# Kernel tuning notes

Hardware: AMD Instinct MI355X
Metric: run time of the kernel (lower is better)

The kernel has to match this reference:

```python
import jax, jax.numpy as jnp
import numpy as np

NUM_TILES = 64
TPC = 8            # tiles per cluster
GRID = 16          # spline grid size
EPS = 1e-5


def setup_inputs() -> dict:
    key = jax.random.key(0)
    ks = jax.random.split(key, 6)
    B, S, D, T, DH, G = 2, 1024, 512, NUM_TILES, 128, GRID
    x = jax.random.normal(ks[0], (B, S, D), dtype=jnp.float32)
    gamma = jnp.ones((D,), jnp.float32)
    beta = jnp.zeros((D,), jnp.float32)
    # torch layouts: down.weight [DH, D], up.weight [D, DH]
    Wd = jax.random.normal(ks[1], (T, DH, D), dtype=jnp.float32) * 0.02
    spline_bases = jax.random.normal(ks[2], (T, DH, G), dtype=jnp.float32) * 0.1
    spline_slopes = jax.random.normal(ks[3], (T, DH, G), dtype=jnp.float32) * 0.1
    Wu = jax.random.normal(ks[4], (T, D, DH), dtype=jnp.float32) * 0.02
    scale = jnp.full((T,), 0.1, jnp.float32)
    return {"x": x, "gamma": gamma, "beta": beta, "Wd": Wd,
            "spline_bases": spline_bases, "spline_slopes": spline_slopes,
            "Wu": Wu, "scale": scale}


def reference(x, gamma, beta, Wd, spline_bases, spline_slopes, Wu, scale):
    B, S, D = x.shape
    T, DH, _ = Wd.shape
    C = T // TPC
    N = B * S

    # LayerNorm
    mu = x.mean(-1, keepdims=True)
    var = ((x - mu) ** 2).mean(-1, keepdims=True)
    xn = (x - mu) * jax.lax.rsqrt(var + EPS) * gamma + beta
    xf = xn.reshape(N, D)

    # Signatures (first call: ema == current tile signatures)
    tile_sigs = jnp.sign(Wd.mean(axis=1))                         # [T, D]
    cluster_sigs = jnp.sign(tile_sigs.reshape(C, TPC, D).mean(1))  # [C, D]

    # Hierarchical routing: cluster -> tile
    in_sigs = jnp.sign(xf)                                        # [N, D]
    best_c = jnp.argmax(in_sigs @ cluster_sigs.T, axis=-1)        # [N]
    tile_scores = (in_sigs @ tile_sigs.T).reshape(N, C, TPC)      # [N, C, TPC]
    sc = jnp.take_along_axis(tile_scores, best_c[:, None, None], axis=1)[:, 0, :]
    local_best = jnp.argmax(sc, axis=-1)                          # [N]
    tidx = best_c * TPC + local_best                              # [N]

    # Dispatch: gather per-token expert weights, down-project
    h = jnp.einsum('nd,nhd->nh', xf, Wd[tidx])                    # [N, DH]

    # Spline nonlinearity
    hn = jax.nn.sigmoid(h)
    idx = jnp.clip((hn * GRID).astype(jnp.int32), 0, GRID - 1)    # [N, DH]
    base = jnp.take_along_axis(spline_bases[tidx], idx[..., None], axis=-1)[..., 0]
    slope = jnp.take_along_axis(spline_slopes[tidx], idx[..., None], axis=-1)[..., 0]
    local_pos = hn * GRID - idx.astype(h.dtype)                   # (hn - idx*cell)/cell
    hs = base + slope * local_pos                                 # [N, DH]

    # Up-project, per-tile scale, combine (dropout is identity in eval)
    y = jnp.einsum('nh,ndh->nd', hs, Wu[tidx]) * scale[tidx][:, None]
    return x + y.reshape(B, S, D)
```

## Files before the change

### kernel.cpp

```cpp
#include <hip/hip_runtime.h>
#include <hip/hip_bf16.h>
#include <math.h>

#define NTILES 64
#define TPC 8
#define NCLUST 8
#define GRID_SZ 16
#define DIM 512
#define DHID 128
#define NTOK 2048
#define LN_EPS 1e-5f
#define TB 16
#define NCHUNK_MAX 192

typedef __attribute__((ext_vector_type(8))) short bf16x8;
typedef __attribute__((ext_vector_type(4))) float f32x4;

static __device__ __forceinline__ float fsign(float v) {
    return (v > 0.f) ? 1.f : ((v < 0.f) ? -1.f : 0.f);
}

static __device__ __forceinline__ unsigned short bf16bits(float f) {
    union { __hip_bfloat16 h; unsigned short s; } u;
    u.h = __float2bfloat16(f);
    return u.s;
}

static __device__ __forceinline__ bf16x8 cvt8(const float* p) {
    float4 a = *(const float4*)p;
    float4 b = *(const float4*)(p + 4);
    float e[8] = {a.x, a.y, a.z, a.w, b.x, b.y, b.z, b.w};
    bf16x8 v;
    #pragma unroll
    for (int i = 0; i < 8; ++i) v[i] = (short)bf16bits(e[i]);
    return v;
}

static __device__ __forceinline__ bool route_chunk(const int* counts, int lane, int cb,
                                                   int& t, int& base, int& m) {
    int cnt_l = counts[lane];
    int nck = (cnt_l + TB - 1) / TB;
    int pre = nck;
    #pragma unroll
    for (int off = 1; off < 64; off <<= 1) {
        int u = __shfl_up(pre, off);
        if (lane >= off) pre += u;
    }
    int total = __shfl(pre, 63);
    pre -= nck;
    if (cb >= total) return false;
    unsigned long long msk = __ballot(cb >= pre && cb < pre + nck);
    t = (int)__builtin_ctzll(msk);
    base = (cb - __shfl(pre, t)) * TB;
    m = min(TB, __shfl(cnt_l, t) - base);
    return true;
}

__global__ __launch_bounds__(256) void k_prep(const float* __restrict__ x,
                                              const float* __restrict__ gamma,
                                              const float* __restrict__ beta,
                                              const float* __restrict__ Wd,
                                              float* __restrict__ psum,
                                              unsigned short* __restrict__ wd_b,
                                              unsigned short* __restrict__ xn_b,
                                              int* __restrict__ counts) {
    int bid = blockIdx.x;
    int tid = threadIdx.x;
    if (bid < 512) {
        int t = bid >> 3, part = bid & 7;
        const float* basep = Wd + ((size_t)t * DHID + part * 16) * DIM;
        unsigned short* bb = wd_b + ((size_t)t * DHID + part * 16) * DIM;
        #pragma unroll
        for (int k2 = 0; k2 < 2; ++k2) {
            int d = tid + k2 * 256;
            float s = 0.f;
            #pragma unroll
            for (int j = 0; j < 16; ++j) {
                float v = basep[(size_t)j * DIM + d];
                s += v;
                bb[(size_t)j * DIM + d] = bf16bits(v);
            }
            psum[((size_t)t * 8 + part) * DIM + d] = s;
        }
        if (bid == 0 && tid < NTILES) counts[tid] = 0;
    } else {
        int n = (bid - 512) * 4 + (tid >> 6);
        int lane = tid & 63;
        const float* xr = x + (size_t)n * DIM;
        float v[8];
        float sum = 0.f;
        #pragma unroll
        for (int j = 0; j < 8; ++j) { float t = xr[lane + 64 * j]; v[j] = t; sum += t; }
        #pragma unroll
        for (int off = 32; off; off >>= 1) sum += __shfl_xor(sum, off);
        float mu = sum * (1.f / DIM);
        float sq = 0.f;
        #pragma unroll
        for (int j = 0; j < 8; ++j) { float t = v[j] - mu; sq += t * t; }
        #pragma unroll
        for (int off = 32; off; off >>= 1) sq += __shfl_xor(sq, off);
        float rs = rsqrtf(sq * (1.f / DIM) + LN_EPS);
        #pragma unroll
        for (int j = 0; j < 8; ++j) {
            int d = lane + 64 * j;
            float xv = (v[j] - mu) * rs * gamma[d] + beta[d];
            xn_b[(size_t)n * DIM + d] = bf16bits(xv);
        }
    }
}

__global__ __launch_bounds__(512) void k_csig(const float* __restrict__ psum,
                                              float* __restrict__ tile_sigs,
                                              float* __restrict__ cluster_sigs) {
    int c = blockIdx.x, d = threadIdx.x;
    float csum = 0.f;
    #pragma unroll
    for (int k = 0; k < TPC; ++k) {
        int t = c * TPC + k;
        float s = 0.f;
        #pragma unroll
        for (int p = 0; p < 8; ++p) s += psum[((size_t)t * 8 + p) * DIM + d];
        float sg = fsign(s);
        tile_sigs[(size_t)t * DIM + d] = sg;
        csum += sg;
    }
    cluster_sigs[(size_t)c * DIM + d] = fsign(csum);
}

__global__ __launch_bounds__(256) void k_route(const unsigned short* __restrict__ xn_b,
                                               const float* __restrict__ tile_sigs,
                                               const float* __restrict__ cluster_sigs,
                                               int* __restrict__ counts,
                                               int* __restrict__ list) {
    int n = blockIdx.x * 4 + (threadIdx.x >> 6);
    int lane = threadIdx.x & 63;
    float sg[8];
    #pragma unroll
    for (int j = 0; j < 8; ++j) {
        unsigned short u = xn_b[(size_t)n * DIM + lane + 64 * j];
        sg[j] = ((u & 0x7fff) == 0) ? 0.f : ((u & 0x8000) ? -1.f : 1.f);
    }
    int best_c = 0; float best = -1e30f;
    for (int c = 0; c < NCLUST; ++c) {
        float s = 0.f;
        #pragma unroll
        for (int j = 0; j < 8; ++j) s += sg[j] * cluster_sigs[(size_t)c * DIM + lane + 64 * j];
        #pragma unroll
        for (int off = 32; off; off >>= 1) s += __shfl_xor(s, off);
        if (s > best) { best = s; best_c = c; }
    }
    int bt = best_c * TPC; float bts = -1e30f;
    for (int k = 0; k < TPC; ++k) {
        int t = best_c * TPC + k;
        float s = 0.f;
        #pragma unroll
        for (int j = 0; j < 8; ++j) s += sg[j] * tile_sigs[(size_t)t * DIM + lane + 64 * j];
        #pragma unroll
        for (int off = 32; off; off >>= 1) s += __shfl_xor(s, off);
        if (s > bts) { bts = s; bt = t; }
    }
    if (lane == 0) {
        int slot = atomicAdd(&counts[bt], 1);
        list[(size_t)bt * NTOK + slot] = n;
    }
}

__global__ __launch_bounds__(512, 2) void k_ffn(const float* __restrict__ x,
                                                const unsigned short* __restrict__ xn_b,
                                                const unsigned short* __restrict__ wd_b,
                                                const float* __restrict__ sb,
                                                const float* __restrict__ ss,
                                                const float* __restrict__ Wu,
                                                const float* __restrict__ scale,
                                                const int* __restrict__ counts,
                                                const int* __restrict__ list,
                                                float* __restrict__ out) {
    int tid = threadIdx.x;
    int lane = tid & 63;
    int wv = tid >> 6;
    int cb = ((int)blockIdx.x & 7) * (NCHUNK_MAX / 8) + ((int)blockIdx.x >> 3);
    int t, base, m;
    if (!route_chunk(counts, lane, cb, t, base, m)) return;

    __shared__ __align__(16) unsigned short hsl[TB * DHID];

    int mrow = lane & 15;
    int ko = (lane >> 4) * 8;
    int tokm = list[(size_t)t * NTOK + base + min(mrow, m - 1)];

    const unsigned short* xr = xn_b + (size_t)tokm * DIM;
    const unsigned short* wr = wd_b + ((size_t)t * DHID + wv * 16 + mrow) * DIM;
    f32x4 acc = {0.f, 0.f, 0.f, 0.f};
    #pragma unroll
    for (int kk = 0; kk < 16; ++kk) {
        int d = kk * 32 + ko;
        bf16x8 a = *(const bf16x8*)(xr + d);
        bf16x8 b = *(const bf16x8*)(wr + d);
        acc = __builtin_amdgcn_mfma_f32_16x16x32_bf16(a, b, acc, 0, 0, 0);
    }
    int dh = wv * 16 + mrow;
    const float* sbt = sb + ((size_t)t * DHID + dh) * GRID_SZ;
    const float* sst = ss + ((size_t)t * DHID + dh) * GRID_SZ;
    #pragma unroll
    for (int r = 0; r < 4; ++r) {
        int tr = (lane >> 4) * 4 + r;
        float h = acc[r];
        float hn = 1.f / (1.f + expf(-h));
        float g = hn * (float)GRID_SZ;
        int idx = (int)g;
        idx = idx > GRID_SZ - 1 ? GRID_SZ - 1 : idx;
        float lp = g - (float)idx;
        float val = sbt[idx] + sst[idx] * lp;
        hsl[(tr * DHID + dh) ^ ((tr & 7) << 3)] = bf16bits(val);
    }
    __syncthreads();

    float sc_t = scale[t];
    bf16x8 a2[4];
    #pragma unroll
    for (int kk = 0; kk < 4; ++kk)
        a2[kk] = *(const bf16x8*)&hsl[(mrow * DHID + kk * 32 + ko) ^ ((mrow & 7) << 3)];
    #pragma unroll
    for (int nt = 0; nt < 4; ++nt) {
        int d = wv * 64 + nt * 16 + mrow;
        const float* wru = Wu + ((size_t)t * DIM + d) * DHID;
        f32x4 au = {0.f, 0.f, 0.f, 0.f};
        #pragma unroll
        for (int kk = 0; kk < 4; ++kk) {
            bf16x8 b = cvt8(wru + kk * 32 + ko);
            au = __builtin_amdgcn_mfma_f32_16x16x32_bf16(a2[kk], b, au, 0, 0, 0);
        }
        #pragma unroll
        for (int r = 0; r < 4; ++r) {
            int tr = (lane >> 4) * 4 + r;
            int tok_tr = __shfl(tokm, tr);
            if (tr < m) {
                size_t o = (size_t)tok_tr * DIM + d;
                out[o] = x[o] + au[r] * sc_t;
            }
        }
    }
}

extern "C" void kernel_launch(void* const* d_in, const int* in_sizes, int n_in,
                              void* d_out, int out_size, void* d_ws, size_t ws_size,
                              hipStream_t stream) {
    const float* x     = (const float*)d_in[0];
    const float* gamma = (const float*)d_in[1];
    const float* beta  = (const float*)d_in[2];
    const float* Wd    = (const float*)d_in[3];
    const float* sb    = (const float*)d_in[4];
    const float* ss    = (const float*)d_in[5];
    const float* Wu    = (const float*)d_in[6];
    const float* scale = (const float*)d_in[7];
    float* out = (float*)d_out;

    float* psum          = (float*)d_ws;
    float* tile_sigs     = psum + (size_t)NTILES * 8 * DIM;
    float* cluster_sigs  = tile_sigs + NTILES * DIM;
    int*   counts        = (int*)(cluster_sigs + NCLUST * DIM);
    int*   list          = counts + NTILES;
    unsigned short* xn_b = (unsigned short*)(list + (size_t)NTILES * NTOK);
    unsigned short* wd_b = xn_b + (size_t)NTOK * DIM;

    k_prep<<<1024, 256, 0, stream>>>(x, gamma, beta, Wd, psum, wd_b, xn_b, counts);
    k_csig<<<NCLUST, 512, 0, stream>>>(psum, tile_sigs, cluster_sigs);
    k_route<<<NTOK / 4, 256, 0, stream>>>(xn_b, tile_sigs, cluster_sigs, counts, list);
    k_ffn<<<NCHUNK_MAX, 512, 0, stream>>>(x, xn_b, wd_b, sb, ss, Wu, scale, counts, list, out);
}
```

Before: 52.13 us.

## Bit-pack sign signatures and route tokens with popcount; split MFMA accumulator chain

Tile and cluster sign signatures are stored as 64-bit ballot bitmasks, with a separate mask marking non-zero cluster entries. Routing then scores every tile at once, one tile per lane, using XOR plus popcount instead of float dot products and sequential wave reductions. The down-projection MFMA loop is also split into two independent accumulators to shorten the dependency chain. Zero-valued token signs are treated as positive bits in the tile score, which can shift scores slightly versus the float path; exact ties now depend on integer ordering.

```diff
diff --git a/kernel.cpp b/kernel.cpp
--- a/kernel.cpp
+++ b/kernel.cpp
@@ -15,10 +15,7 @@
 
 typedef __attribute__((ext_vector_type(8))) short bf16x8;
 typedef __attribute__((ext_vector_type(4))) float f32x4;
-
-static __device__ __forceinline__ float fsign(float v) {
-    return (v > 0.f) ? 1.f : ((v < 0.f) ? -1.f : 0.f);
-}
+typedef unsigned long long u64;
 
 static __device__ __forceinline__ unsigned short bf16bits(float f) {
     union { __hip_bfloat16 h; unsigned short s; } u;
@@ -49,7 +46,7 @@
     int total = __shfl(pre, 63);
     pre -= nck;
     if (cb >= total) return false;
-    unsigned long long msk = __ballot(cb >= pre && cb < pre + nck);
+    u64 msk = __ballot(cb >= pre && cb < pre + nck);
     t = (int)__builtin_ctzll(msk);
     base = (cb - __shfl(pre, t)) * TB;
     m = min(TB, __shfl(cnt_l, t) - base);
@@ -110,54 +107,72 @@
 }
 
 __global__ __launch_bounds__(512) void k_csig(const float* __restrict__ psum,
-                                              float* __restrict__ tile_sigs,
-                                              float* __restrict__ cluster_sigs) {
-    int c = blockIdx.x, d = threadIdx.x;
-    float csum = 0.f;
-    #pragma unroll
-    for (int k = 0; k < TPC; ++k) {
-        int t = c * TPC + k;
+                                              u64* __restrict__ tbits,
+                                              u64* __restrict__ cbits,
+                                              u64* __restrict__ cmask) {
+    int c = blockIdx.x;
+    int w = threadIdx.x >> 6;
+    int lane = threadIdx.x & 63;
+    int t = c * TPC + w;
+    __shared__ u64 tb_lds[TPC][8];
+    #pragma unroll
+    for (int j = 0; j < 8; ++j) {
+        int d = lane + 64 * j;
         float s = 0.f;
         #pragma unroll
         for (int p = 0; p < 8; ++p) s += psum[((size_t)t * 8 + p) * DIM + d];
-        float sg = fsign(s);
-        tile_sigs[(size_t)t * DIM + d] = sg;
-        csum += sg;
-    }
-    cluster_sigs[(size_t)c * DIM + d] = fsign(csum);
+        u64 b = __ballot(s < 0.f);
+        if (lane == 0) { tbits[t * 8 + j] = b; tb_lds[w][j] = b; }
+    }
+    __syncthreads();
+    int cnt = 0;
+    #pragma unroll
+    for (int k = 0; k < TPC; ++k) cnt += (int)((tb_lds[k][w] >> lane) & 1ULL);
+    u64 cb = __ballot(cnt > 4);
+    u64 cm = __ballot(cnt != 4);
+    if (lane == 0) { cbits[c * 8 + w] = cb; cmask[c * 8 + w] = cm; }
 }
 
 __global__ __launch_bounds__(256) void k_route(const unsigned short* __restrict__ xn_b,
-                                               const float* __restrict__ tile_sigs,
-                                               const float* __restrict__ cluster_sigs,
+                                               const u64* __restrict__ tbits,
+                                               const u64* __restrict__ cbits,
+                                               const u64* __restrict__ cmask,
                                                int* __restrict__ counts,
                                                int* __restrict__ list) {
     int n = blockIdx.x * 4 + (threadIdx.x >> 6);
     int lane = threadIdx.x & 63;
-    float sg[8];
+    u64 xb[8];
     #pragma unroll
     for (int j = 0; j < 8; ++j) {
         unsigned short u = xn_b[(size_t)n * DIM + lane + 64 * j];
-        sg[j] = ((u & 0x7fff) == 0) ? 0.f : ((u & 0x8000) ? -1.f : 1.f);
-    }
-    int best_c = 0; float best = -1e30f;
-    for (int c = 0; c < NCLUST; ++c) {
-        float s = 0.f;
-        #pragma unroll
-        for (int j = 0; j < 8; ++j) s += sg[j] * cluster_sigs[(size_t)c * DIM + lane + 64 * j];
-        #pragma unroll
-        for (int off = 32; off; off >>= 1) s += __shfl_xor(s, off);
-        if (s > best) { best = s; best_c = c; }
-    }
-    int bt = best_c * TPC; float bts = -1e30f;
-    for (int k = 0; k < TPC; ++k) {
-        int t = best_c * TPC + k;
-        float s = 0.f;
-        #pragma unroll
-        for (int j = 0; j < 8; ++j) s += sg[j] * tile_sigs[(size_t)t * DIM + lane + 64 * j];
-        #pragma unroll
-        for (int off = 32; off; off >>= 1) s += __shfl_xor(s, off);
-        if (s > bts) { bts = s; bt = t; }
+        xb[j] = __ballot((u & 0x8000u) != 0 && (u & 0x7fffu) != 0);
+    }
+    const u64* tb = tbits + lane * 8;
+    int ts = 0;
+    #pragma unroll
+    for (int j = 0; j < 8; ++j) ts += __popcll(xb[j] ^ tb[j]);
+    int tscore = DIM - 2 * ts;
+    int cscore = -(1 << 30);
+    if (lane < NCLUST) {
+        const u64* cb = cbits + lane * 8;
+        const u64* cm = cmask + lane * 8;
+        int s = 0;
+        #pragma unroll
+        for (int j = 0; j < 8; ++j)
+            s += __popcll(cm[j]) - 2 * __popcll((xb[j] ^ cb[j]) & cm[j]);
+        cscore = s;
+    }
+    int bc = 0, best = __shfl(cscore, 0);
+    #pragma unroll
+    for (int k = 1; k < NCLUST; ++k) {
+        int v = __shfl(cscore, k);
+        if (v > best) { best = v; bc = k; }
+    }
+    int bt = bc * TPC, bts = __shfl(tscore, bc * TPC);
+    #pragma unroll
+    for (int k = 1; k < TPC; ++k) {
+        int v = __shfl(tscore, bc * TPC + k);
+        if (v > bts) { bts = v; bt = bc * TPC + k; }
     }
     if (lane == 0) {
         int slot = atomicAdd(&counts[bt], 1);
@@ -190,14 +205,19 @@
 
     const unsigned short* xr = xn_b + (size_t)tokm * DIM;
     const unsigned short* wr = wd_b + ((size_t)t * DHID + wv * 16 + mrow) * DIM;
-    f32x4 acc = {0.f, 0.f, 0.f, 0.f};
-    #pragma unroll
-    for (int kk = 0; kk < 16; ++kk) {
-        int d = kk * 32 + ko;
-        bf16x8 a = *(const bf16x8*)(xr + d);
-        bf16x8 b = *(const bf16x8*)(wr + d);
-        acc = __builtin_amdgcn_mfma_f32_16x16x32_bf16(a, b, acc, 0, 0, 0);
-    }
+    f32x4 acc0 = {0.f, 0.f, 0.f, 0.f}, acc1 = acc0;
+    #pragma unroll
+    for (int kk = 0; kk < 8; ++kk) {
+        int d0 = kk * 32 + ko;
+        int d1 = (kk + 8) * 32 + ko;
+        bf16x8 a0 = *(const bf16x8*)(xr + d0);
+        bf16x8 b0 = *(const bf16x8*)(wr + d0);
+        acc0 = __builtin_amdgcn_mfma_f32_16x16x32_bf16(a0, b0, acc0, 0, 0, 0);
+        bf16x8 a1 = *(const bf16x8*)(xr + d1);
+        bf16x8 b1 = *(const bf16x8*)(wr + d1);
+        acc1 = __builtin_amdgcn_mfma_f32_16x16x32_bf16(a1, b1, acc1, 0, 0, 0);
+    }
+    f32x4 acc = acc0 + acc1;
     int dh = wv * 16 + mrow;
     const float* sbt = sb + ((size_t)t * DHID + dh) * GRID_SZ;
     const float* sst = ss + ((size_t)t * DHID + dh) * GRID_SZ;
@@ -256,15 +276,16 @@
     float* out = (float*)d_out;
 
     float* psum          = (float*)d_ws;
-    float* tile_sigs     = psum + (size_t)NTILES * 8 * DIM;
-    float* cluster_sigs  = tile_sigs + NTILES * DIM;
-    int*   counts        = (int*)(cluster_sigs + NCLUST * DIM);
+    u64*   tbits         = (u64*)(psum + (size_t)NTILES * 8 * DIM);
+    u64*   cbits         = tbits + NTILES * 8;
+    u64*   cmask         = cbits + NCLUST * 8;
+    int*   counts        = (int*)(cmask + NCLUST * 8);
     int*   list          = counts + NTILES;
     unsigned short* xn_b = (unsigned short*)(list + (size_t)NTILES * NTOK);
     unsigned short* wd_b = xn_b + (size_t)NTOK * DIM;
 
     k_prep<<<1024, 256, 0, stream>>>(x, gamma, beta, Wd, psum, wd_b, xn_b, counts);
-    k_csig<<<NCLUST, 512, 0, stream>>>(psum, tile_sigs, cluster_sigs);
-    k_route<<<NTOK / 4, 256, 0, stream>>>(xn_b, tile_sigs, cluster_sigs, counts, list);
+    k_csig<<<NCLUST, 512, 0, stream>>>(psum, tbits, cbits, cmask);
+    k_route<<<NTOK / 4, 256, 0, stream>>>(xn_b, tbits, cbits, cmask, counts, list);
     k_ffn<<<NCHUNK_MAX, 512, 0, stream>>>(x, xn_b, wd_b, sb, ss, Wu, scale, counts, list, out);
 }
```

Measured after the change: 51.38 us. About the same (-1.4%).
